# Kernel optimization log

Measured on AMD Instinct MI355X. Metric: run time of the kernel, lower is better.

The kernel has to match this reference:

```python
import jax, jax.numpy as jnp
import numpy as np
from jax import lax

B, S, V, E, H, L = 256, 512, 32, 128, 512, 4  # batch, seq, vocab, embed, rnn_units, layers


def _lstm_bias(n4h):
    # Keras unit_forget_bias=True: forget-gate slice initialized to 1.
    b = jnp.zeros((n4h,), jnp.float32)
    return b.at[n4h // 4: n4h // 2].set(1.0)


def setup_inputs() -> dict:
    key = jax.random.key(0)
    ks = jax.random.split(key, 10)
    g = lambda k, shape, sc=0.02: (jax.random.normal(k, shape, jnp.float32) * sc)
    return dict(
        tokens=jax.random.randint(ks[0], (B, S), 0, V),
        emb=g(ks[1], (V, E), 0.05),
        w0=g(ks[2], (E, 4 * H)),
        u0=g(ks[3], (H, 4 * H)),
        b0=_lstm_bias(4 * H),
        w_rest=g(ks[4], (L - 1, H, 4 * H)),
        u_rest=g(ks[5], (L - 1, H, 4 * H)),
        b_rest=jnp.tile(_lstm_bias(4 * H)[None], (L - 1, 1)),
        dw1=g(ks[6], (H, 2 * H)),
        db1=jnp.zeros((2 * H,), jnp.float32),
        dw2=g(ks[7], (2 * H, V)),
        db2=jnp.zeros((V,), jnp.float32),
    )


def _lstm_layer(x, W, U, b):
    # x: [B,S,D]. Precompute input projection once (big GEMM), scan the recurrence.
    xz = jnp.einsum('bsd,dk->bsk', x, W) + b  # [B,S,4H]
    h0 = jnp.zeros((x.shape[0], H), x.dtype)
    c0 = jnp.zeros_like(h0)

    def step(carry, z_t):
        h, c = carry
        z = z_t + h @ U                      # [B,4H]
        i, f, g, o = jnp.split(z, 4, axis=-1)  # Keras gate order i,f,c,o
        i = jax.nn.sigmoid(i)
        f = jax.nn.sigmoid(f)
        g = jnp.tanh(g)
        o = jax.nn.sigmoid(o)
        c = f * c + i * g
        h = o * jnp.tanh(c)
        return (h, c), h

    _, hs = lax.scan(step, (h0, c0), jnp.swapaxes(xz, 0, 1))  # time-major scan
    return jnp.swapaxes(hs, 0, 1)  # [B,S,H]


def reference(tokens, emb, w0, u0, b0, w_rest, u_rest, b_rest, dw1, db1, dw2, db2):
    x = emb[tokens] * jnp.sqrt(jnp.float32(E))  # embedding scaled by sqrt(embedding_dim)
    x = _lstm_layer(x, w0, u0, b0)
    for i in range(L - 1):  # fixed small layer loop
        x = _lstm_layer(x, w_rest[i], u_rest[i], b_rest[i])
    h = jax.nn.relu(jnp.einsum('bsh,hk->bsk', x, dw1) + db1)
    return jnp.einsum('bsk,kv->bsv', h, dw2) + db2  # logits [B,S,V]
```

## Files before the change

kernel.cpp:

```cpp
#include <hip/hip_runtime.h>
#include <stdint.h>

#define NB 256
#define NS 512
#define NV 32
#define NE 128
#define NH 512
#define N4H 2048

typedef __attribute__((ext_vector_type(8))) short short8;
typedef __attribute__((ext_vector_type(4))) float f32x4;
typedef __attribute__((ext_vector_type(4))) unsigned int u32x4;
typedef __attribute__((ext_vector_type(4))) unsigned short u16x4;

__device__ __forceinline__ float bf2f(unsigned short u){
  unsigned int x = ((unsigned int)u) << 16;
  return __builtin_bit_cast(float, x);
}
__device__ __forceinline__ unsigned short f2bf(float f){
  unsigned int u = __builtin_bit_cast(unsigned int, f);
  u += 0x7fffu + ((u >> 16) & 1u);
  return (unsigned short)(u >> 16);
}
__device__ __forceinline__ void gload_lds16(const void* g, void* l){
  __builtin_amdgcn_global_load_lds(
      (const __attribute__((address_space(1))) unsigned int*)(uintptr_t)g,
      (__attribute__((address_space(3))) unsigned int*)(uintptr_t)l,
      16, 0, 0);
}

__global__ __launch_bounds__(256) void transpose_cast(
    const float* __restrict__ in, unsigned short* __restrict__ out, int K, int N)
{
  int k = blockIdx.x * 256 + threadIdx.x;
  int n = blockIdx.y;
  if (k < K) out[(long)n * K + k] = f2bf(in[(long)k * N + n]);
}

__global__ __launch_bounds__(256) void embed_kernel(
    const int* __restrict__ tok, const float* __restrict__ emb,
    unsigned short* __restrict__ x0)
{
  long gid = (long)blockIdx.x * 256 + threadIdx.x;
  long idx = gid * 4;
  int e = (int)(idx & 127);
  int b = (int)((idx >> 7) & 255);
  int t = (int)(idx >> 15);
  int tk = tok[b * NS + t];
  f32x4 v = *(const f32x4*)(emb + (long)tk * NE + e);
  u16x4 o;
  #pragma unroll
  for (int i = 0; i < 4; ++i) o[i] = f2bf(v[i] * 11.313708498984761f);
  *(u16x4*)(x0 + idx) = o;
}

template<int BM, int BN, bool BIAS, bool RELU, bool F32OUT, bool REMAP>
__global__ __launch_bounds__(256) void gemm_bt(
    const unsigned short* __restrict__ A, const unsigned short* __restrict__ BT,
    void* __restrict__ Cv, const float* __restrict__ bias,
    int M, int N, int K, int rowoff)
{
  constexpr int BK = 64;
  constexpr int WN = (BN >= 64) ? 2 : 1;
  constexpr int WM = 4 / WN;
  constexpr int WTM = BM / WM, WTN = BN / WN;
  constexpr int FM = WTM / 16, FN = WTN / 16;
  __shared__ unsigned short lds[(BM + BN) * BK];
  unsigned short* As = lds;
  unsigned short* Bs = lds + BM * BK;
  const int tid = threadIdx.x;
  const int w = tid >> 6, l = tid & 63;
  const int n0 = blockIdx.x * BN, m0 = blockIdx.y * BM;
  const int wm = (WN == 2) ? (w >> 1) : w;
  const int wn = (WN == 2) ? (w & 1) : 0;

  f32x4 acc[FM][FN];
  #pragma unroll
  for (int i = 0; i < FM; i++)
    #pragma unroll
    for (int j = 0; j < FN; j++) acc[i][j] = (f32x4)0.f;

  constexpr int CH_A = BM * 8;
  constexpr int CH_T = (BM + BN) * 8;
  constexpr int PW = CH_T / 4;
  static_assert(PW % 64 == 0, "staging alignment");
  static_assert(CH_A % 64 == 0, "region boundary alignment");

  for (int kt = 0; kt < K; kt += BK) {
    #pragma unroll
    for (int i = 0; i < PW / 64; ++i) {
      int c0 = w * PW + i * 64;
      int c = c0 + l;
      const unsigned short* g;
      if (c0 < CH_A) {
        int row = c >> 3, col = c & 7;
        g = A + (long)(m0 + row) * K + kt + col * 8;
      } else {
        int cb = c - CH_A;
        int row = cb >> 3, col = cb & 7;
        g = BT + (long)(n0 + row) * K + kt + col * 8;
      }
      gload_lds16(g, lds + (size_t)c0 * 8);
    }
    __syncthreads();
    #pragma unroll
    for (int ks = 0; ks < BK / 32; ++ks) {
      short8 a[FM], b[FN];
      #pragma unroll
      for (int mt = 0; mt < FM; ++mt)
        a[mt] = *(const short8*)&As[(wm * WTM + mt * 16 + (l & 15)) * BK + ks * 32 + (l >> 4) * 8];
      #pragma unroll
      for (int nt = 0; nt < FN; ++nt)
        b[nt] = *(const short8*)&Bs[(wn * WTN + nt * 16 + (l & 15)) * BK + ks * 32 + (l >> 4) * 8];
      #pragma unroll
      for (int mt = 0; mt < FM; ++mt)
        #pragma unroll
        for (int nt = 0; nt < FN; ++nt)
          acc[mt][nt] = __builtin_amdgcn_mfma_f32_16x16x32_bf16(a[mt], b[nt], acc[mt][nt], 0, 0, 0);
    }
    __syncthreads();
  }

  const int row_l = l >> 4, col_l = l & 15;
  #pragma unroll
  for (int nt = 0; nt < FN; ++nt) {
    int col = n0 + wn * WTN + nt * 16 + col_l;
    float bv = 0.f;
    if (BIAS) bv = bias[col];
    #pragma unroll
    for (int mt = 0; mt < FM; ++mt) {
      #pragma unroll
      for (int i = 0; i < 4; ++i) {
        int m = m0 + wm * WTM + mt * 16 + row_l * 4 + i;
        float v = acc[mt][nt][i] + bv;
        if (RELU) v = v > 0.f ? v : 0.f;
        long cidx;
        if (REMAP) {
          int gr = rowoff + m;
          int b_ = gr & (NB - 1), t_ = gr >> 8;
          cidx = ((long)b_ * NS + t_) * N + col;
        } else {
          cidx = (long)m * N + col;
        }
        if (F32OUT) ((float*)Cv)[cidx] = v;
        else ((unsigned short*)Cv)[cidx] = f2bf(v);
      }
    }
  }
}

#define SC_LDS_U 65536
#define SC_LDS_H (16 * 32 * 80)
#define SC_LDS_Z (32 * 65 * 4)
#define SCAN_LDS_BYTES (SC_LDS_U + SC_LDS_H + SC_LDS_Z)

template<int KD>
__global__ __launch_bounds__(256) void lstm_scan_fused(
    const unsigned short* __restrict__ x_in,
    const unsigned short* __restrict__ WT,
    const unsigned short* __restrict__ UT,
    const float* __restrict__ bias,
    unsigned short* __restrict__ x_out,
    unsigned short* __restrict__ h_buf,
    unsigned int* __restrict__ seq)
{
  constexpr int KS = KD / 32;
  extern __shared__ char smem[];
  unsigned short* Uf = (unsigned short*)smem;
  char* Ha = smem + SC_LDS_U;
  float* Zl = (float*)(smem + SC_LDS_U + SC_LDS_H);
  const int tid = threadIdx.x, w = tid >> 6, l = tid & 63;
  const int group = blockIdx.x & 7;
  const int slice = blockIdx.x >> 3;
  const int u0 = slice * 16;

  for (int idx = tid; idx < 4096; idx += 256) {
    int ll = idx & 63, nt = (idx >> 6) & 3, ks = idx >> 8;
    int gc = nt * NH + u0 + (ll & 15);
    int kb = ks * 32 + (ll >> 4) * 8;
    u32x4 v = *(const u32x4*)(UT + (size_t)gc * NH + kb);
    *(u32x4*)((char*)Uf + (size_t)idx * 16) = v;
  }

  const int j2 = tid & 15;
  const int r0 = tid >> 4;
  const int n_ = u0 + j2;
  const int brow0 = group * 32 + r0;
  const float bv = bias[w * NH + u0 + (l & 15)];
  float c_state[2] = {0.f, 0.f};
  const int hwo = group * 16384 + (n_ >> 5) * 1024 + (n_ & 31);
  unsigned int* seqg = seq + group * 32;
  unsigned int* myseq = seqg + slice;
  const int ownlane = ((l & 31) == slice);
  const unsigned short* xr0 = x_in + (size_t)(group * 32 + (l & 15)) * KD + (l >> 4) * 8;
  const unsigned short* wp  = WT + (size_t)(w * NH + u0 + (l & 15)) * KD + (l >> 4) * 8;

  __syncthreads();

  for (int t = 0; t < NS; ++t) {
    f32x4 acc0 = {bv, bv, bv, bv}, acc1 = {bv, bv, bv, bv};
    {
      const unsigned short* xa = xr0 + (size_t)t * NB * KD;
      #pragma unroll
      for (int ks = 0; ks < KS; ++ks) {
        short8 a0 = *(const short8*)(xa + ks * 32);
        short8 a1 = *(const short8*)(xa + (size_t)16 * KD + ks * 32);
        short8 bw = *(const short8*)(wp + ks * 32);
        acc0 = __builtin_amdgcn_mfma_f32_16x16x32_bf16(a0, bw, acc0, 0, 0, 0);
        acc1 = __builtin_amdgcn_mfma_f32_16x16x32_bf16(a1, bw, acc1, 0, 0, 0);
      }
    }
    if (t > 0) {
      {
        const unsigned int* fp = seqg + (l & 31);
        unsigned int v; int spin = 0;
        do {
          asm volatile("global_load_dword %0, %1, off sc0 sc1\n\ts_waitcnt vmcnt(0)"
                       : "=v"(v) : "v"(fp) : "memory");
        } while (!__all((int)(v >= (unsigned)t) | ownlane) && ++spin < (1 << 14));
      }
      const unsigned short* hsrc = h_buf + (size_t)((t - 1) & 1) * 131072 + group * 16384;
      u32x4 hv[8];
      #pragma unroll
      for (int i = 0; i < 8; ++i) {
        const unsigned short* gp = hsrc + (size_t)(tid + i * 256) * 8;
        asm volatile("global_load_dwordx4 %0, %1, off sc0 sc1"
                     : "=v"(hv[i]) : "v"(gp) : "memory");
      }
      asm volatile("s_waitcnt vmcnt(0)" ::: "memory");
      __builtin_amdgcn_sched_barrier(0);
      #pragma unroll
      for (int i = 0; i < 8; ++i) {
        int g = tid + i * 256;
        int ks = g >> 7, rem = g & 127, rr = rem >> 2, cq = rem & 3;
        *(u32x4*)(Ha + ks * 2560 + rr * 80 + cq * 16) = hv[i];
      }
      __syncthreads();
      #pragma unroll
      for (int ks = 0; ks < 16; ++ks) {
        short8 bfr = *(const short8*)((char*)Uf + ((size_t)(ks * 4 + w) * 64 + l) * 16);
        short8 a0 = *(const short8*)(Ha + ks * 2560 + (l & 15) * 80 + (l >> 4) * 16);
        short8 a1 = *(const short8*)(Ha + ks * 2560 + ((l & 15) + 16) * 80 + (l >> 4) * 16);
        acc0 = __builtin_amdgcn_mfma_f32_16x16x32_bf16(a0, bfr, acc0, 0, 0, 0);
        acc1 = __builtin_amdgcn_mfma_f32_16x16x32_bf16(a1, bfr, acc1, 0, 0, 0);
      }
    }
    #pragma unroll
    for (int i = 0; i < 4; ++i) {
      Zl[((l >> 4) * 4 + i) * 65 + w * 16 + (l & 15)] = acc0[i];
      Zl[((l >> 4) * 4 + i + 16) * 65 + w * 16 + (l & 15)] = acc1[i];
    }
    __syncthreads();
    unsigned short hb2[2];
    #pragma unroll
    for (int p = 0; p < 2; ++p) {
      int r = r0 + p * 16;
      float zi = Zl[r * 65 +      j2];
      float zf = Zl[r * 65 + 16 + j2];
      float zg = Zl[r * 65 + 32 + j2];
      float zo = Zl[r * 65 + 48 + j2];
      float ig = 1.f / (1.f + __expf(-zi));
      float fg = 1.f / (1.f + __expf(-zf));
      float gg = 1.f - 2.f / (__expf(2.f * zg) + 1.f);
      float og = 1.f / (1.f + __expf(-zo));
      float c = fg * c_state[p] + ig * gg;
      c_state[p] = c;
      float th = 1.f - 2.f / (__expf(2.f * c) + 1.f);
      hb2[p] = f2bf(og * th);
    }
    {
      unsigned short* hd = h_buf + (size_t)(t & 1) * 131072 + hwo;
      unsigned int v0 = hb2[0], v1 = hb2[1];
      asm volatile("global_store_short %0, %1, off sc0 sc1"
                   :: "v"(hd + r0 * 32), "v"(v0) : "memory");
      asm volatile("global_store_short %0, %1, off sc0 sc1"
                   :: "v"(hd + (r0 + 16) * 32), "v"(v1) : "memory");
      asm volatile("s_waitcnt vmcnt(0)" ::: "memory");
    }
    __syncthreads();
    if (tid == 0) {
      unsigned int nv = (unsigned int)(t + 1);
      asm volatile("global_store_dword %0, %1, off sc0 sc1"
                   :: "v"(myseq), "v"(nv) : "memory");
    }
    x_out[((size_t)t * NB + brow0) * NH + n_] = hb2[0];
    x_out[((size_t)t * NB + brow0 + 16) * NH + n_] = hb2[1];
  }
}

extern "C" void kernel_launch(void* const* d_in, const int* in_sizes, int n_in,
                              void* d_out, int out_size, void* d_ws, size_t ws_size,
                              hipStream_t stream) {
  const int*   tokens = (const int*)  d_in[0];
  const float* emb    = (const float*)d_in[1];
  const float* w0     = (const float*)d_in[2];
  const float* u0     = (const float*)d_in[3];
  const float* b0     = (const float*)d_in[4];
  const float* w_rest = (const float*)d_in[5];
  const float* u_rest = (const float*)d_in[6];
  const float* b_rest = (const float*)d_in[7];
  const float* dw1    = (const float*)d_in[8];
  const float* db1    = (const float*)d_in[9];
  const float* dw2    = (const float*)d_in[10];
  const float* db2    = (const float*)d_in[11];
  float* out = (float*)d_out;

  char* ws = (char*)d_ws;
  size_t off = 0;
  auto alloc = [&](size_t bytes) -> char* {
    char* p = ws + off;
    off += (bytes + 255) & ~(size_t)255;
    return p;
  };
  unsigned short* ut[4];
  for (int i = 0; i < 4; ++i) ut[i] = (unsigned short*)alloc((size_t)N4H * NH * 2);
  unsigned short* w0t = (unsigned short*)alloc((size_t)N4H * NE * 2);
  unsigned short* wt[3];
  for (int i = 0; i < 3; ++i) wt[i] = (unsigned short*)alloc((size_t)N4H * NH * 2);
  unsigned short* dw1t = (unsigned short*)alloc((size_t)1024 * 512 * 2);
  unsigned short* dw2t = (unsigned short*)alloc((size_t)32 * 1024 * 2);
  unsigned short* x0  = (unsigned short*)alloc((size_t)NB * NS * NE * 2);
  unsigned short* xA  = (unsigned short*)alloc((size_t)NB * NS * NH * 2);
  unsigned short* hb  = (unsigned short*)alloc((size_t)2 * 8 * 16384 * 2);
  unsigned int*  seq  = (unsigned int*)alloc((size_t)4 * 8 * 32 * 4);

  size_t avail = (ws_size > off) ? (ws_size - off) : 0;
  long RC = (long)(avail / ((size_t)1024 * 2));
  if (RC > (long)NB * NS) RC = (long)NB * NS;
  RC &= ~(long)127;
  if (RC < 128) RC = 128;
  unsigned short* h1buf = (unsigned short*)alloc((size_t)RC * 1024 * 2);

  (void)hipMemsetAsync(seq, 0, (size_t)4 * 8 * 32 * 4, stream);

  transpose_cast<<<dim3(1, N4H), 256, 0, stream>>>(w0, w0t, NE, N4H);
  transpose_cast<<<dim3(2, N4H), 256, 0, stream>>>(u0, ut[0], NH, N4H);
  for (int i = 0; i < 3; ++i) {
    transpose_cast<<<dim3(2, N4H), 256, 0, stream>>>(w_rest + (size_t)i * NH * N4H, wt[i], NH, N4H);
    transpose_cast<<<dim3(2, N4H), 256, 0, stream>>>(u_rest + (size_t)i * NH * N4H, ut[i + 1], NH, N4H);
  }
  transpose_cast<<<dim3(2, 1024), 256, 0, stream>>>(dw1, dw1t, 512, 1024);
  transpose_cast<<<dim3(4, 32), 256, 0, stream>>>(dw2, dw2t, 1024, 32);

  embed_kernel<<<16384, 256, 0, stream>>>(tokens, emb, x0);

  (void)hipFuncSetAttribute((const void*)lstm_scan_fused<NE>,
                            hipFuncAttributeMaxDynamicSharedMemorySize, SCAN_LDS_BYTES);
  (void)hipFuncSetAttribute((const void*)lstm_scan_fused<NH>,
                            hipFuncAttributeMaxDynamicSharedMemorySize, SCAN_LDS_BYTES);

  lstm_scan_fused<NE><<<256, 256, SCAN_LDS_BYTES, stream>>>(
      x0, w0t, ut[0], b0, xA, hb, seq);
  for (int lyr = 1; lyr < 4; ++lyr) {
    lstm_scan_fused<NH><<<256, 256, SCAN_LDS_BYTES, stream>>>(
        xA, wt[lyr - 1], ut[lyr], b_rest + (size_t)(lyr - 1) * N4H, xA, hb,
        seq + (size_t)lyr * 8 * 32);
  }

  for (long r0 = 0; r0 < (long)NB * NS; r0 += RC) {
    long rows = ((long)NB * NS - r0 < RC) ? ((long)NB * NS - r0) : RC;
    gemm_bt<128, 128, true, true, false, false>
        <<<dim3(1024 / 128, rows / 128), 256, 0, stream>>>(
            xA + (size_t)r0 * NH, dw1t, h1buf, db1, (int)rows, 1024, NH, 0);
    gemm_bt<128, 32, true, false, true, true>
        <<<dim3(1, rows / 128), 256, 0, stream>>>(
            h1buf, dw2t, out, db2, (int)rows, 32, 1024, (int)r0);
  }
}
```

Baseline: 11.56 ms.

## Warp-specialize LSTM scan: register-resident weights, overlapped input projection, atomic step counter

Each 4-wave block of the LSTM scan is split by role. Waves 0-1 compute the input projection for step t and prefetch x for t+1 into registers. Waves 2-3 do only the recurrent h·U product, with U fragments and h operands held in registers rather than staged through LDS. The per-slice sequence flags are replaced by one atomic counter per group. The h broadcast and x_out stores are deferred to the next iteration and handled by dedicated waves. This aims to shorten the serial per-step critical path and hide the input GEMM and stores behind the recurrence, at the cost of very high register pressure (possible spills) and more atomic traffic on one counter.

```diff
diff --git a/kernel.cpp b/kernel.cpp
--- a/kernel.cpp
+++ b/kernel.cpp
@@ -149,142 +149,172 @@
   }
 }
 
-#define SC_LDS_U 65536
-#define SC_LDS_H (16 * 32 * 80)
-#define SC_LDS_Z (32 * 65 * 4)
-#define SCAN_LDS_BYTES (SC_LDS_U + SC_LDS_H + SC_LDS_Z)
-
 template<int KD>
-__global__ __launch_bounds__(256) void lstm_scan_fused(
+__global__ __launch_bounds__(256, 1) void lstm_scan_fused(
     const unsigned short* __restrict__ x_in,
     const unsigned short* __restrict__ WT,
     const unsigned short* __restrict__ UT,
     const float* __restrict__ bias,
     unsigned short* __restrict__ x_out,
     unsigned short* __restrict__ h_buf,
-    unsigned int* __restrict__ seq)
+    unsigned int* __restrict__ cnt)
 {
   constexpr int KS = KD / 32;
-  extern __shared__ char smem[];
-  unsigned short* Uf = (unsigned short*)smem;
-  char* Ha = smem + SC_LDS_U;
-  float* Zl = (float*)(smem + SC_LDS_U + SC_LDS_H);
-  const int tid = threadIdx.x, w = tid >> 6, l = tid & 63;
+  __shared__ float Zlx[32 * 65];
+  __shared__ float Zlh[32 * 65];
+  __shared__ unsigned short hpack[32 * 16];
+
+  const int tid = threadIdx.x, wv = tid >> 6, l = tid & 63;
   const int group = blockIdx.x & 7;
   const int slice = blockIdx.x >> 3;
   const int u0 = slice * 16;
-
-  for (int idx = tid; idx < 4096; idx += 256) {
-    int ll = idx & 63, nt = (idx >> 6) & 3, ks = idx >> 8;
-    int gc = nt * NH + u0 + (ll & 15);
-    int kb = ks * 32 + (ll >> 4) * 8;
-    u32x4 v = *(const u32x4*)(UT + (size_t)gc * NH + kb);
-    *(u32x4*)((char*)Uf + (size_t)idx * 16) = v;
-  }
-
-  const int j2 = tid & 15;
-  const int r0 = tid >> 4;
-  const int n_ = u0 + j2;
-  const int brow0 = group * 32 + r0;
-  const float bv = bias[w * NH + u0 + (l & 15)];
-  float c_state[2] = {0.f, 0.f};
-  const int hwo = group * 16384 + (n_ >> 5) * 1024 + (n_ & 31);
-  unsigned int* seqg = seq + group * 32;
-  unsigned int* myseq = seqg + slice;
-  const int ownlane = ((l & 31) == slice);
-  const unsigned short* xr0 = x_in + (size_t)(group * 32 + (l & 15)) * KD + (l >> 4) * 8;
-  const unsigned short* wp  = WT + (size_t)(w * NH + u0 + (l & 15)) * KD + (l >> 4) * 8;
-
+  const int lr = l & 15, lk = l >> 4;
+  const int j2 = tid & 15, r0 = tid >> 4;
+  const int wz = wv & 1;
+
+  short8 wfrag[2][16];
+  float bv0 = 0.f, bv1 = 0.f;
+  if (wv < 2) {
+    #pragma unroll
+    for (int g = 0; g < 2; ++g)
+      #pragma unroll
+      for (int ks = 0; ks < KS; ++ks)
+        wfrag[g][ks] = *(const short8*)(WT + (size_t)((2 * wz + g) * NH + u0 + lr) * KD + ks * 32 + lk * 8);
+    bv0 = bias[(2 * wz + 0) * NH + u0 + lr];
+    bv1 = bias[(2 * wz + 1) * NH + u0 + lr];
+  } else {
+    #pragma unroll
+    for (int g = 0; g < 2; ++g)
+      #pragma unroll
+      for (int ks = 0; ks < 16; ++ks)
+        wfrag[g][ks] = *(const short8*)(UT + (size_t)((2 * wz + g) * NH + u0 + lr) * NH + ks * 32 + lk * 8);
+  }
+
+  short8 xa[2][16];
+  const unsigned short* xp0 = x_in + (size_t)(group * 32 + lr) * KD + lk * 8;
+  if (wv < 2) {
+    #pragma unroll
+    for (int m = 0; m < 2; ++m)
+      #pragma unroll
+      for (int ks = 0; ks < KS; ++ks)
+        xa[m][ks] = *(const short8*)(xp0 + (size_t)m * 16 * KD + ks * 32);
+  }
+
+  unsigned short* hd0 = h_buf + group * 16384 + (slice >> 1) * 1024 + (slice & 1) * 16
+                        + (l >> 1) * 32 + (l & 1) * 8;
+  unsigned short* xo0 = x_out + (size_t)(group * 32 + (l >> 1)) * NH + u0 + (l & 1) * 8;
+  const unsigned short* hb0 = h_buf + group * 16384 + lr * 32 + lk * 8;
+  unsigned int* cp = cnt + group * 16;
+  const unsigned int one = 1u;
+
+  for (int i = tid; i < 32 * 65; i += 256) Zlh[i] = 0.f;
   __syncthreads();
 
+  float c0 = 0.f, c1 = 0.f;
+
   for (int t = 0; t < NS; ++t) {
-    f32x4 acc0 = {bv, bv, bv, bv}, acc1 = {bv, bv, bv, bv};
-    {
-      const unsigned short* xa = xr0 + (size_t)t * NB * KD;
+    if (wv == 0) {
+      if (t > 0) {
+        u32x4 hv = *(const u32x4*)((const char*)hpack + l * 16);
+        unsigned short* hd = hd0 + (size_t)((t - 1) & 1) * 131072;
+        asm volatile("global_store_dwordx4 %0, %1, off sc0 sc1"
+                     :: "v"(hd), "v"(hv) : "memory");
+        asm volatile("s_waitcnt vmcnt(0)" ::: "memory");
+        if (l == 0)
+          asm volatile("global_atomic_add %0, %1, off sc1"
+                       :: "v"(cp), "v"(one) : "memory");
+      }
+    } else if (wv == 1) {
+      if (t > 0) {
+        u32x4 hv = *(const u32x4*)((const char*)hpack + l * 16);
+        *(u32x4*)(xo0 + (size_t)(t - 1) * NB * NH) = hv;
+      }
+    }
+
+    if (wv < 2) {
+      f32x4 a00 = {bv0, bv0, bv0, bv0}, a01 = {bv0, bv0, bv0, bv0};
+      f32x4 a10 = {bv1, bv1, bv1, bv1}, a11 = {bv1, bv1, bv1, bv1};
       #pragma unroll
       for (int ks = 0; ks < KS; ++ks) {
-        short8 a0 = *(const short8*)(xa + ks * 32);
-        short8 a1 = *(const short8*)(xa + (size_t)16 * KD + ks * 32);
-        short8 bw = *(const short8*)(wp + ks * 32);
-        acc0 = __builtin_amdgcn_mfma_f32_16x16x32_bf16(a0, bw, acc0, 0, 0, 0);
-        acc1 = __builtin_amdgcn_mfma_f32_16x16x32_bf16(a1, bw, acc1, 0, 0, 0);
-      }
-    }
-    if (t > 0) {
+        a00 = __builtin_amdgcn_mfma_f32_16x16x32_bf16(xa[0][ks], wfrag[0][ks], a00, 0, 0, 0);
+        a01 = __builtin_amdgcn_mfma_f32_16x16x32_bf16(xa[1][ks], wfrag[0][ks], a01, 0, 0, 0);
+        a10 = __builtin_amdgcn_mfma_f32_16x16x32_bf16(xa[0][ks], wfrag[1][ks], a10, 0, 0, 0);
+        a11 = __builtin_amdgcn_mfma_f32_16x16x32_bf16(xa[1][ks], wfrag[1][ks], a11, 0, 0, 0);
+      }
+      #pragma unroll
+      for (int i = 0; i < 4; ++i) {
+        Zlx[(lk * 4 + i) * 65      + (2 * wz + 0) * 16 + lr] = a00[i];
+        Zlx[(16 + lk * 4 + i) * 65 + (2 * wz + 0) * 16 + lr] = a01[i];
+        Zlx[(lk * 4 + i) * 65      + (2 * wz + 1) * 16 + lr] = a10[i];
+        Zlx[(16 + lk * 4 + i) * 65 + (2 * wz + 1) * 16 + lr] = a11[i];
+      }
+      int tn = (t + 1 < NS) ? (t + 1) : t;
+      const unsigned short* xp = xp0 + (size_t)tn * NB * KD;
+      #pragma unroll
+      for (int m = 0; m < 2; ++m)
+        #pragma unroll
+        for (int ks = 0; ks < KS; ++ks)
+          xa[m][ks] = *(const short8*)(xp + (size_t)m * 16 * KD + ks * 32);
+    } else if (t > 0) {
       {
-        const unsigned int* fp = seqg + (l & 31);
-        unsigned int v; int spin = 0;
+        unsigned int v, target = 32u * (unsigned)t;
+        int spin = 0;
         do {
           asm volatile("global_load_dword %0, %1, off sc0 sc1\n\ts_waitcnt vmcnt(0)"
-                       : "=v"(v) : "v"(fp) : "memory");
-        } while (!__all((int)(v >= (unsigned)t) | ownlane) && ++spin < (1 << 14));
-      }
-      const unsigned short* hsrc = h_buf + (size_t)((t - 1) & 1) * 131072 + group * 16384;
-      u32x4 hv[8];
-      #pragma unroll
-      for (int i = 0; i < 8; ++i) {
-        const unsigned short* gp = hsrc + (size_t)(tid + i * 256) * 8;
+                       : "=v"(v) : "v"(cp) : "memory");
+        } while (v < target && ++spin < (1 << 15));
+      }
+      const unsigned short* hb_ = hb0 + (size_t)((t - 1) & 1) * 131072;
+      short8 ha[2][16];
+      #pragma unroll
+      for (int ks = 0; ks < 16; ++ks) {
         asm volatile("global_load_dwordx4 %0, %1, off sc0 sc1"
-                     : "=v"(hv[i]) : "v"(gp) : "memory");
+                     : "=v"(ha[0][ks]) : "v"(hb_ + ks * 1024) : "memory");
+        asm volatile("global_load_dwordx4 %0, %1, off sc0 sc1"
+                     : "=v"(ha[1][ks]) : "v"(hb_ + ks * 1024 + 512) : "memory");
       }
       asm volatile("s_waitcnt vmcnt(0)" ::: "memory");
       __builtin_amdgcn_sched_barrier(0);
-      #pragma unroll
-      for (int i = 0; i < 8; ++i) {
-        int g = tid + i * 256;
-        int ks = g >> 7, rem = g & 127, rr = rem >> 2, cq = rem & 3;
-        *(u32x4*)(Ha + ks * 2560 + rr * 80 + cq * 16) = hv[i];
-      }
-      __syncthreads();
+      f32x4 a00 = (f32x4)0.f, a01 = (f32x4)0.f, a10 = (f32x4)0.f, a11 = (f32x4)0.f;
       #pragma unroll
       for (int ks = 0; ks < 16; ++ks) {
-        short8 bfr = *(const short8*)((char*)Uf + ((size_t)(ks * 4 + w) * 64 + l) * 16);
-        short8 a0 = *(const short8*)(Ha + ks * 2560 + (l & 15) * 80 + (l >> 4) * 16);
-        short8 a1 = *(const short8*)(Ha + ks * 2560 + ((l & 15) + 16) * 80 + (l >> 4) * 16);
-        acc0 = __builtin_amdgcn_mfma_f32_16x16x32_bf16(a0, bfr, acc0, 0, 0, 0);
-        acc1 = __builtin_amdgcn_mfma_f32_16x16x32_bf16(a1, bfr, acc1, 0, 0, 0);
-      }
-    }
-    #pragma unroll
-    for (int i = 0; i < 4; ++i) {
-      Zl[((l >> 4) * 4 + i) * 65 + w * 16 + (l & 15)] = acc0[i];
-      Zl[((l >> 4) * 4 + i + 16) * 65 + w * 16 + (l & 15)] = acc1[i];
+        a00 = __builtin_amdgcn_mfma_f32_16x16x32_bf16(ha[0][ks], wfrag[0][ks], a00, 0, 0, 0);
+        a01 = __builtin_amdgcn_mfma_f32_16x16x32_bf16(ha[1][ks], wfrag[0][ks], a01, 0, 0, 0);
+        a10 = __builtin_amdgcn_mfma_f32_16x16x32_bf16(ha[0][ks], wfrag[1][ks], a10, 0, 0, 0);
+        a11 = __builtin_amdgcn_mfma_f32_16x16x32_bf16(ha[1][ks], wfrag[1][ks], a11, 0, 0, 0);
+      }
+      #pragma unroll
+      for (int i = 0; i < 4; ++i) {
+        Zlh[(lk * 4 + i) * 65      + (2 * wz + 0) * 16 + lr] = a00[i];
+        Zlh[(16 + lk * 4 + i) * 65 + (2 * wz + 0) * 16 + lr] = a01[i];
+        Zlh[(lk * 4 + i) * 65      + (2 * wz + 1) * 16 + lr] = a10[i];
+        Zlh[(16 + lk * 4 + i) * 65 + (2 * wz + 1) * 16 + lr] = a11[i];
+      }
     }
     __syncthreads();
-    unsigned short hb2[2];
+
     #pragma unroll
     for (int p = 0; p < 2; ++p) {
       int r = r0 + p * 16;
-      float zi = Zl[r * 65 +      j2];
-      float zf = Zl[r * 65 + 16 + j2];
-      float zg = Zl[r * 65 + 32 + j2];
-      float zo = Zl[r * 65 + 48 + j2];
+      float zi = Zlx[r * 65 +      j2] + Zlh[r * 65 +      j2];
+      float zf = Zlx[r * 65 + 16 + j2] + Zlh[r * 65 + 16 + j2];
+      float zg = Zlx[r * 65 + 32 + j2] + Zlh[r * 65 + 32 + j2];
+      float zo = Zlx[r * 65 + 48 + j2] + Zlh[r * 65 + 48 + j2];
       float ig = 1.f / (1.f + __expf(-zi));
       float fg = 1.f / (1.f + __expf(-zf));
       float gg = 1.f - 2.f / (__expf(2.f * zg) + 1.f);
       float og = 1.f / (1.f + __expf(-zo));
-      float c = fg * c_state[p] + ig * gg;
-      c_state[p] = c;
-      float th = 1.f - 2.f / (__expf(2.f * c) + 1.f);
-      hb2[p] = f2bf(og * th);
-    }
-    {
-      unsigned short* hd = h_buf + (size_t)(t & 1) * 131072 + hwo;
-      unsigned int v0 = hb2[0], v1 = hb2[1];
-      asm volatile("global_store_short %0, %1, off sc0 sc1"
-                   :: "v"(hd + r0 * 32), "v"(v0) : "memory");
-      asm volatile("global_store_short %0, %1, off sc0 sc1"
-                   :: "v"(hd + (r0 + 16) * 32), "v"(v1) : "memory");
-      asm volatile("s_waitcnt vmcnt(0)" ::: "memory");
+      float cc = fg * (p ? c1 : c0) + ig * gg;
+      if (p) c1 = cc; else c0 = cc;
+      float th = 1.f - 2.f / (__expf(2.f * cc) + 1.f);
+      hpack[r * 16 + j2] = f2bf(og * th);
     }
     __syncthreads();
-    if (tid == 0) {
-      unsigned int nv = (unsigned int)(t + 1);
-      asm volatile("global_store_dword %0, %1, off sc0 sc1"
-                   :: "v"(myseq), "v"(nv) : "memory");
-    }
-    x_out[((size_t)t * NB + brow0) * NH + n_] = hb2[0];
-    x_out[((size_t)t * NB + brow0 + 16) * NH + n_] = hb2[1];
+  }
+
+  if (wv == 1) {
+    u32x4 hv = *(const u32x4*)((const char*)hpack + l * 16);
+    *(u32x4*)(xo0 + (size_t)(NS - 1) * NB * NH) = hv;
   }
 }
 
@@ -322,7 +352,7 @@
   unsigned short* x0  = (unsigned short*)alloc((size_t)NB * NS * NE * 2);
   unsigned short* xA  = (unsigned short*)alloc((size_t)NB * NS * NH * 2);
   unsigned short* hb  = (unsigned short*)alloc((size_t)2 * 8 * 16384 * 2);
-  unsigned int*  seq  = (unsigned int*)alloc((size_t)4 * 8 * 32 * 4);
+  unsigned int*  cnt  = (unsigned int*)alloc((size_t)4 * 8 * 16 * 4);
 
   size_t avail = (ws_size > off) ? (ws_size - off) : 0;
   long RC = (long)(avail / ((size_t)1024 * 2));
@@ -331,7 +361,7 @@
   if (RC < 128) RC = 128;
   unsigned short* h1buf = (unsigned short*)alloc((size_t)RC * 1024 * 2);
 
-  (void)hipMemsetAsync(seq, 0, (size_t)4 * 8 * 32 * 4, stream);
+  (void)hipMemsetAsync(cnt, 0, (size_t)4 * 8 * 16 * 4, stream);
 
   transpose_cast<<<dim3(1, N4H), 256, 0, stream>>>(w0, w0t, NE, N4H);
   transpose_cast<<<dim3(2, N4H), 256, 0, stream>>>(u0, ut[0], NH, N4H);
@@ -344,17 +374,12 @@
 
   embed_kernel<<<16384, 256, 0, stream>>>(tokens, emb, x0);
 
-  (void)hipFuncSetAttribute((const void*)lstm_scan_fused<NE>,
-                            hipFuncAttributeMaxDynamicSharedMemorySize, SCAN_LDS_BYTES);
-  (void)hipFuncSetAttribute((const void*)lstm_scan_fused<NH>,
-                            hipFuncAttributeMaxDynamicSharedMemorySize, SCAN_LDS_BYTES);
-
-  lstm_scan_fused<NE><<<256, 256, SCAN_LDS_BYTES, stream>>>(
-      x0, w0t, ut[0], b0, xA, hb, seq);
+  lstm_scan_fused<NE><<<256, 256, 0, stream>>>(
+      x0, w0t, ut[0], b0, xA, hb, cnt);
   for (int lyr = 1; lyr < 4; ++lyr) {
-    lstm_scan_fused<NH><<<256, 256, SCAN_LDS_BYTES, stream>>>(
+    lstm_scan_fused<NH><<<256, 256, 0, stream>>>(
         xA, wt[lyr - 1], ut[lyr], b_rest + (size_t)(lyr - 1) * N4H, xA, hb,
-        seq + (size_t)lyr * 8 * 32);
+        cnt + (size_t)lyr * 8 * 16);
   }
 
   for (long r0 = 0; r0 < (long)NB * NS; r0 += RC) {
```

After: 13.95 ms. 20.7% more time.
